# Performance work log

Hardware: AMD Instinct MI355X
Metric: run time of the kernel (lower is better)

The kernel has to match this reference:

```python
import jax, jax.numpy as jnp
import numpy as np

LAYER_SPECS = [(2, 4, 1), (2, 4, 1), (1, 4, 1), (1, 4, 1)]
SKIPS = [(k - s) * d for (s, k, d) in LAYER_SPECS]  # (ksz-stride)*dilation
C = 80  # encoder channels


def _conv1d(x, w, b, stride, dilation):
    # x: (N, Cin, L), w: (Cout, Cin, K)
    out = jax.lax.conv_general_dilated(
        x, w, window_strides=(stride,), padding='VALID',
        rhs_dilation=(dilation,), dimension_numbers=('NCH', 'OIH', 'NCH'))
    return out + b[None, :, None]


def _encoder(x, w_wide, b_wide, w_1x1, b_1x1, w_f0, b_f0, w_f1, b_f1):
    # x: (N, T, 80) -> (N, T', 80)
    x = jnp.transpose(x, (0, 2, 1))  # (N, 80, T)
    for i, ((stride, ksz, dil), skip) in enumerate(zip(LAYER_SPECS, SKIPS)):
        x1 = _conv1d(x, w_wide[i], b_wide[i], stride, dil)  # (N, 2C, L')
        a, g = jnp.split(x1, 2, axis=1)
        x2 = jnp.tanh(a) * jax.nn.sigmoid(g)                # gated activation
        x3 = _conv1d(x2, w_1x1[i], b_1x1[i], 1, 1)          # (N, C, L')
        if i == 0:
            x = x3
        else:
            T3 = x3.shape[2]
            # residual: strided slice of previous x, take last of each stride group
            res = x[:, :, skip:skip + T3 * stride].reshape(x.shape[0], C, T3, stride)[:, :, :, -1]
            x = x3 + res
    x = _conv1d(jax.nn.relu(_conv1d(x, w_f0, b_f0, 1, 1)), w_f1, b_f1, 1, 1)
    return jnp.transpose(x, (0, 2, 1))  # (N, T', 80)


def setup_inputs() -> dict:
    key = jax.random.key(0)
    ks = jax.random.split(key, 10)
    N, Ts, Tq = 16, 8192, 2048
    return {
        'search': jax.random.normal(ks[0], (N, Ts, 80), dtype=jnp.float32),
        'query': jax.random.normal(ks[1], (N, Tq, 80), dtype=jnp.float32),
        'w_wide': jax.random.normal(ks[2], (4, 160, 80, 4), dtype=jnp.float32) * 0.02,
        'b_wide': jnp.zeros((4, 160), dtype=jnp.float32),
        'w_1x1': jax.random.normal(ks[3], (4, 80, 80, 1), dtype=jnp.float32) * 0.05,
        'b_1x1': jnp.zeros((4, 80), dtype=jnp.float32),
        'w_f0': jax.random.normal(ks[4], (80, 80, 1), dtype=jnp.float32) * 0.05,
        'b_f0': jnp.zeros((80,), dtype=jnp.float32),
        'w_f1': jax.random.normal(ks[5], (80, 80, 1), dtype=jnp.float32) * 0.05,
        'b_f1': jax.random.normal(ks[6], (80,), dtype=jnp.float32) * 0.05,
        'embedding': jax.random.normal(ks[7], (1, 512, 80), dtype=jnp.float32) * 0.001,
        'w_lin': jax.random.normal(ks[8], (2, 80), dtype=jnp.float32) * 0.05,
        'b_lin': jnp.zeros((2,), dtype=jnp.float32),
    }


def reference(search, query, w_wide, b_wide, w_1x1, b_1x1,
              w_f0, b_f0, w_f1, b_f1, embedding, w_lin, b_lin):
    enc_s = _encoder(search, w_wide, b_wide, w_1x1, b_1x1, w_f0, b_f0, w_f1, b_f1)
    enc_q = _encoder(query, w_wide, b_wide, w_1x1, b_1x1, w_f0, b_f0, w_f1, b_f1)

    # ---- VectorQuant (no normalize): nearest-codeword lookup + straight-through ----
    x = enc_s[:, :, None, :]                  # (N, T, 1, V)
    N, T, nc, V = x.shape
    n_classes = embedding.shape[1]
    x1 = x.reshape(N * T, nc, V)              # (NT, 1, V)
    # squared-distance via expansion: argmin identical to argmin of L2 norm
    x2 = jnp.sum(x1 * x1, axis=-1, keepdims=True)          # (NT, 1, 1)
    e2 = jnp.sum(embedding * embedding, axis=-1)[None]     # (1, 1, K)
    xe = jnp.einsum('ncv,ckv->nck', x1, embedding)         # (NT, 1, K)
    idx = jnp.argmin(x2 - 2.0 * xe + e2, axis=2)           # (NT, 1)
    offset = jnp.arange(nc) * n_classes
    flat = embedding.reshape(-1, V)
    output = flat[(idx + offset[None, :]).reshape(-1)].reshape(x.shape)
    out0 = jax.lax.stop_gradient(output - x) + x           # straight-through
    discrete = out0[:, :, 0, :]               # (N, Ts', V)

    # ---- align query to search length, classify, max-pool over time ----
    sf = discrete.shape[1] // enc_q.shape[1]
    q = jnp.tile(enc_q, (1, sf, 1))
    pad = discrete.shape[1] - q.shape[1]
    q = jnp.pad(q, ((0, 0), (0, pad), (0, 0)))
    pred = jnp.tanh((q + discrete) @ w_lin.T + b_lin)      # (N, Ts', 2)
    return jnp.max(pred, axis=1)                           # (N, 2)
```

## Files before the change

kernel.cpp:

```cpp
#include <hip/hip_runtime.h>
#include <math.h>


#define NBATCH 16

typedef __attribute__((ext_vector_type(8))) short s16x8;
typedef __attribute__((ext_vector_type(4))) float f32x4;

__device__ __forceinline__ float fast_sigmoid(float x){ return 1.0f/(1.0f+__expf(-x)); }
__device__ __forceinline__ float fast_tanh(float x){ return 2.0f/(1.0f+__expf(-2.0f*x))-1.0f; }
__device__ __forceinline__ unsigned short f2bf(float f){
    unsigned int u = __float_as_uint(f);
    return (unsigned short)((u + 0x7FFFu + ((u >> 16) & 1u)) >> 16);
}

__global__ __launch_bounds__(256) void pack_all(
    const float* __restrict__ w_wide, const float* __restrict__ w_1x1,
    const float* __restrict__ wf0,    const float* __restrict__ wf1,
    const float* __restrict__ emb,
    unsigned short* __restrict__ WW, unsigned short* __restrict__ W1,
    unsigned short* __restrict__ F0, unsigned short* __restrict__ F1,
    unsigned short* __restrict__ EM, float* __restrict__ e2o)
{
    int i = blockIdx.x * 256 + threadIdx.x;
    if (i < 204800) {
        int l = i / 51200, r = i % 51200, oc = r / 320, k = r % 320;
        int j = k / 80, ic = k % 80;
        WW[i] = f2bf(w_wide[l * 51200 + oc * 320 + ic * 4 + j]);
    } else if (i < 235520) {
        int idx = i - 204800, l = idx / 7680, r = idx % 7680, oc = r / 96, k = r % 96;
        W1[idx] = (k < 80) ? f2bf(w_1x1[l * 6400 + oc * 80 + k]) : (unsigned short)0;
    } else if (i < 243200) {
        int idx = i - 235520, oc = idx / 96, k = idx % 96;
        F0[idx] = (k < 80) ? f2bf(wf0[oc * 80 + k]) : (unsigned short)0;
    } else if (i < 250880) {
        int idx = i - 243200, oc = idx / 96, k = idx % 96;
        F1[idx] = (k < 80) ? f2bf(wf1[oc * 80 + k]) : (unsigned short)0;
    } else if (i < 291840) {
        EM[i - 250880] = f2bf(emb[i - 250880]);
    } else if (i < 292352) {
        int e = i - 291840;
        float s = 0.f;
        for (int k = 0; k < 80; ++k) { float v = emb[e * 80 + k]; s = fmaf(v, v, s); }
        e2o[e] = s;
    }
}

template<int S, bool HAS_RES, bool FINAL>
__global__ __launch_bounds__(320, 6) void enc_layer(
    const float* __restrict__ xS, const float* __restrict__ xQ,
    const unsigned short* __restrict__ ww,  const float* __restrict__ wb,
    const unsigned short* __restrict__ w1p, const float* __restrict__ b1,
    const unsigned short* __restrict__ f0p, const float* __restrict__ bf0,
    const unsigned short* __restrict__ f1p, const float* __restrict__ bf1,
    float* __restrict__ outS, float* __restrict__ outQ,
    int TinS, int ToutS, int TinQ, int ToutQ, int nbS)
{
    constexpr int TILE = 32;
    constexpr int MT   = 2;
    constexpr int P    = (TILE - 1) * S + 4;
    constexpr int HALF = (S == 2) ? (P / 2) : P;
    constexpr int NEL  = P * 20;
    constexpr int NST  = (NEL + 319) / 320;
    constexpr int NPARY = (S == 2) ? 2 : 1;

    __shared__ __attribute__((aligned(16))) unsigned short xs[NPARY * HALF * 88];
    __shared__ __attribute__((aligned(16))) unsigned short gsA[TILE * 104];
    __shared__ __attribute__((aligned(16))) unsigned short gsB[FINAL ? TILE * 104 : 8];

    const int tid  = threadIdx.x;
    const int wave = tid >> 6;
    const int lane = tid & 63;
    const int m    = lane & 15;
    const int quad = lane >> 4;
    const int n_   = blockIdx.y;

    const float* x; float* out; int T_in, T_out, bx;
    if ((int)blockIdx.x < nbS) { x = xS; out = outS; T_in = TinS; T_out = ToutS; bx = blockIdx.x; }
    else                       { x = xQ; out = outQ; T_in = TinQ; T_out = ToutQ; bx = blockIdx.x - nbS; }
    const int t0 = bx * TILE;
    const long base_in = (long)n_ * T_in * 80;

    const int quad8 = quad * 8;
    const unsigned short* wa_base = ww + (long)(wave * 16 + m) * 320 + quad8;
    const unsigned short* wg_base = ww + (long)((wave + 5) * 16 + m) * 320 + quad8;
    auto ldB = [&](const unsigned short* b, int kk) { return *(const s16x8*)(b + kk * 32); };

    float4 vst[NST]; int odx[NST]; bool okw[NST];
#pragma unroll
    for (int it = 0; it < NST; ++it) {
        int u = tid + it * 320;
        okw[it] = (u < NEL);
        if (u >= NEL) u = NEL - 1;
        int pos = u / 20, c4 = u % 20;
        int tp = t0 * S + pos; if (tp > T_in - 1) tp = T_in - 1;
        vst[it] = *(const float4*)(x + base_in + (long)tp * 80 + c4 * 4);
        int row = (S == 2) ? (pos >> 1) : pos;
        int par = (S == 2) ? (pos & 1) : 0;
        odx[it] = (par * HALF + row) * 88 + c4 * 4;
    }

    s16x8 baP[3], bgP[3];
    baP[0] = ldB(wa_base, 0); bgP[0] = ldB(wg_base, 0);
    baP[1] = ldB(wa_base, 1); bgP[1] = ldB(wg_base, 1);

#pragma unroll
    for (int it = 0; it < NST; ++it) {
        if (okw[it]) {
            float4 v = vst[it];
            unsigned int s0 = (unsigned int)f2bf(v.x) | ((unsigned int)f2bf(v.y) << 16);
            unsigned int s1 = (unsigned int)f2bf(v.z) | ((unsigned int)f2bf(v.w) << 16);
            *(uint2*)&xs[odx[it]] = make_uint2(s0, s1);
        }
    }

    f32x4 acc_a[MT], acc_g[MT];
#pragma unroll
    for (int mt = 0; mt < MT; ++mt) {
        acc_a[mt] = (f32x4){0.f, 0.f, 0.f, 0.f};
        acc_g[mt] = (f32x4){0.f, 0.f, 0.f, 0.f};
    }

    __syncthreads();

#pragma unroll
    for (int kk = 0; kk < 10; ++kk) {
        if (kk + 2 < 10) {
            baP[(kk + 2) % 3] = ldB(wa_base, kk + 2);
            bgP[(kk + 2) % 3] = ldB(wg_base, kk + 2);
        }
        const int kq = kk * 32 + quad8;
        const int j  = (kq >= 240) ? 3 : ((kq >= 160) ? 2 : ((kq >= 80) ? 1 : 0));
        const int ic0 = kq - j * 80;
        int xb;
        if (S == 2) xb = ((j & 1) * HALF + (j >> 1)) * 88 + ic0;
        else        xb = j * 88 + ic0;
        s16x8 a[MT];
#pragma unroll
        for (int mt = 0; mt < MT; ++mt)
            a[mt] = *(const s16x8*)&xs[xb + (mt * 16 + m) * 88];
        s16x8 ba = baP[kk % 3], bg = bgP[kk % 3];
#pragma unroll
        for (int mt = 0; mt < MT; ++mt) {
            acc_a[mt] = __builtin_amdgcn_mfma_f32_16x16x32_bf16(a[mt], ba, acc_a[mt], 0, 0, 0);
            acc_g[mt] = __builtin_amdgcn_mfma_f32_16x16x32_bf16(a[mt], bg, acc_g[mt], 0, 0, 0);
        }
    }

    const float ba_b = wb[wave * 16 + m];
    const float bg_b = wb[80 + wave * 16 + m];
#pragma unroll
    for (int mt = 0; mt < MT; ++mt)
#pragma unroll
        for (int r = 0; r < 4; ++r) {
            float av = acc_a[mt][r] + ba_b;
            float gv = acc_g[mt][r] + bg_b;
            gsA[(mt * 16 + quad * 4 + r) * 104 + wave * 16 + m] =
                f2bf(fast_tanh(av) * fast_sigmoid(gv));
        }
    const uint4 z4 = make_uint4(0u, 0u, 0u, 0u);
    {
        constexpr int NPAD = FINAL ? 128 : 64;
        for (int u = tid; u < NPAD; u += 320) {
            unsigned short* g = (u < 64) ? gsA : gsB;
            int v = u & 63;
            *(uint4*)&g[(v >> 1) * 104 + 80 + (v & 1) * 8] = z4;
        }
    }
    __syncthreads();

    auto mm96 = [&](const unsigned short* Wp, const unsigned short* g, f32x4 (&o)[MT]) {
        const unsigned short* wb1 = Wp + (long)(wave * 16 + m) * 96 + quad8;
        s16x8 b0  = *(const s16x8*)(wb1);
        s16x8 b1f = *(const s16x8*)(wb1 + 32);
        s16x8 b2  = *(const s16x8*)(wb1 + 64);
#pragma unroll
        for (int mt = 0; mt < MT; ++mt) o[mt] = (f32x4){0.f, 0.f, 0.f, 0.f};
#pragma unroll
        for (int kb = 0; kb < 3; ++kb) {
            s16x8 b = (kb == 0) ? b0 : ((kb == 1) ? b1f : b2);
#pragma unroll
            for (int mt = 0; mt < MT; ++mt) {
                s16x8 ag = *(const s16x8*)&g[(mt * 16 + m) * 104 + kb * 32 + quad8];
                o[mt] = __builtin_amdgcn_mfma_f32_16x16x32_bf16(ag, b, o[mt], 0, 0, 0);
            }
        }
    };

    f32x4 a1[MT];
    mm96(w1p, gsA, a1);

    const long base_out = (long)n_ * T_out * 80;
    const int c = wave * 16 + m;
    if (!FINAL) {
        const float b1c = b1[c];
#pragma unroll
        for (int mt = 0; mt < MT; ++mt)
#pragma unroll
            for (int r = 0; r < 4; ++r) {
                int tg = t0 + mt * 16 + quad * 4 + r;
                if (tg < T_out) {
                    float v = a1[mt][r] + b1c;
                    if (HAS_RES)
                        v += x[base_in + (long)(3 + (long)tg * S) * 80 + c];
                    out[base_out + (long)tg * 80 + c] = v;
                }
            }
    } else {
        const float b1c = b1[c];
        float x3[MT][4];
#pragma unroll
        for (int mt = 0; mt < MT; ++mt)
#pragma unroll
            for (int r = 0; r < 4; ++r) {
                int tg = t0 + mt * 16 + quad * 4 + r;
                int tc = (tg < T_out) ? tg : (T_out - 1);
                float v = a1[mt][r] + b1c;
                if (HAS_RES)
                    v += x[base_in + (long)(3 + (long)tc * S) * 80 + c];
                x3[mt][r] = v;
            }
#pragma unroll
        for (int mt = 0; mt < MT; ++mt)
#pragma unroll
            for (int r = 0; r < 4; ++r)
                gsB[(mt * 16 + quad * 4 + r) * 104 + c] = f2bf(x3[mt][r]);
        __syncthreads();
        f32x4 a2[MT];
        mm96(f0p, gsB, a2);
        const float bf0c = bf0[c];
#pragma unroll
        for (int mt = 0; mt < MT; ++mt)
#pragma unroll
            for (int r = 0; r < 4; ++r)
                gsA[(mt * 16 + quad * 4 + r) * 104 + c] =
                    f2bf(fmaxf(a2[mt][r] + bf0c, 0.f));
        __syncthreads();
        f32x4 a3[MT];
        mm96(f1p, gsA, a3);
        const float bf1c = bf1[c];
#pragma unroll
        for (int mt = 0; mt < MT; ++mt)
#pragma unroll
            for (int r = 0; r < 4; ++r) {
                int tg = t0 + mt * 16 + quad * 4 + r;
                if (tg < T_out)
                    out[base_out + (long)tg * 80 + c] = a3[mt][r] + bf1c;
            }
    }
}

__global__ __launch_bounds__(256, 2) void vq_mfma(
    const float* __restrict__ enc_s, const float* __restrict__ enc_q,
    const unsigned short* __restrict__ embp, const float* __restrict__ emb,
    const float* __restrict__ e2v,
    const float* __restrict__ w_lin, const float* __restrict__ b_lin,
    float* __restrict__ pred)
{
    __shared__ unsigned short xs[64 * 104];
    __shared__ unsigned short es[128 * 104];
    const uint4 z4 = make_uint4(0u, 0u, 0u, 0u);

    const int tid  = threadIdx.x;
    const int wave = tid >> 6;
    const int lane = tid & 63;
    const int m    = lane & 15;
    const int quad = lane >> 4;
    const int n    = blockIdx.y;
    const int t0   = blockIdx.x * 64;

    for (int u = tid; u < 64 * 20; u += 256) {
        int row = u / 20, c4 = u % 20;
        int t = t0 + row; if (t > 2039) t = 2039;
        float4 v = *(const float4*)(enc_s + ((long)n * 2040 + t) * 80 + c4 * 4);
        unsigned int s0 = (unsigned int)f2bf(v.x) | ((unsigned int)f2bf(v.y) << 16);
        unsigned int s1 = (unsigned int)f2bf(v.z) | ((unsigned int)f2bf(v.w) << 16);
        *(uint2*)&xs[row * 104 + c4 * 4] = make_uint2(s0, s1);
    }
    for (int u = tid; u < 128; u += 256)
        *(uint4*)&xs[(u >> 1) * 104 + 80 + (u & 1) * 8] = z4;
    __syncthreads();

    s16x8 af[3];
#pragma unroll
    for (int kb = 0; kb < 3; ++kb)
        af[kb] = *(const s16x8*)&xs[(wave * 16 + m) * 104 + kb * 32 + quad * 8];

    float best[4]; int bi[4];
#pragma unroll
    for (int r = 0; r < 4; ++r) { best[r] = 1e30f; bi[r] = 0; }

    for (int ch = 0; ch < 4; ++ch) {
        const int c0 = ch * 128;
        __syncthreads();
        for (int u = tid; u < 128 * 12; u += 256) {
            int el = u / 12, seg = u % 12;
            uint4 v = z4;
            if (seg < 10) v = *(const uint4*)(embp + (long)(c0 + el) * 80 + seg * 8);
            *(uint4*)&es[el * 104 + seg * 8] = v;
        }
        __syncthreads();

        f32x4 acc[8];
#pragma unroll
        for (int nt = 0; nt < 8; ++nt) acc[nt] = (f32x4){0.f, 0.f, 0.f, 0.f};
#pragma unroll
        for (int kb = 0; kb < 3; ++kb) {
            const int k0 = kb * 32 + quad * 8;
#pragma unroll
            for (int nt = 0; nt < 8; ++nt) {
                s16x8 b = *(const s16x8*)&es[(nt * 16 + m) * 104 + k0];
                acc[nt] = __builtin_amdgcn_mfma_f32_16x16x32_bf16(af[kb], b, acc[nt], 0, 0, 0);
            }
        }
#pragma unroll
        for (int nt = 0; nt < 8; ++nt) {
            const int e = c0 + nt * 16 + m;
            const float e2x = e2v[e];
#pragma unroll
            for (int r = 0; r < 4; ++r) {
                float s = fmaf(-2.0f, acc[nt][r], e2x);
                if (s < best[r]) { best[r] = s; bi[r] = e; }
            }
        }
    }

    __syncthreads();
    float* rb = (float*)es;
    int*   ri = (int*)es + 1088;
#pragma unroll
    for (int r = 0; r < 4; ++r) {
        int tl = wave * 16 + quad * 4 + r;
        rb[tl * 17 + m] = best[r];
        ri[tl * 17 + m] = bi[r];
    }
    __syncthreads();

    if (tid < 64) {
        const int t = t0 + tid;
        float b = rb[tid * 17]; int ix = ri[tid * 17];
#pragma unroll
        for (int j = 1; j < 16; ++j) {
            float v = rb[tid * 17 + j]; int iv = ri[tid * 17 + j];
            if (v < b || (v == b && iv < ix)) { b = v; ix = iv; }
        }
        if (t < 2040) {
            const float4* ev = (const float4*)(emb + (long)ix * 80);
            const bool hasq = (t < 2016);
            const float4* qv = hasq
                ? (const float4*)(enc_q + ((long)n * 504 + (t % 504)) * 80) : nullptr;
            float p0 = b_lin[0], p1 = b_lin[1];
#pragma unroll
            for (int i = 0; i < 20; ++i) {
                float4 e4 = ev[i];
                float4 q4 = hasq ? qv[i] : make_float4(0.f, 0.f, 0.f, 0.f);
                float4 w0 = *(const float4*)(w_lin + 4 * i);
                float4 w1 = *(const float4*)(w_lin + 80 + 4 * i);
                float sx = e4.x + q4.x, sy = e4.y + q4.y;
                float sz = e4.z + q4.z, sw = e4.w + q4.w;
                p0 = fmaf(sx, w0.x, p0); p1 = fmaf(sx, w1.x, p1);
                p0 = fmaf(sy, w0.y, p0); p1 = fmaf(sy, w1.y, p1);
                p0 = fmaf(sz, w0.z, p0); p1 = fmaf(sz, w1.z, p1);
                p0 = fmaf(sw, w0.w, p0); p1 = fmaf(sw, w1.w, p1);
            }
            long o = ((long)n * 2040 + t) * 2;
            pred[o]     = fast_tanh(p0);
            pred[o + 1] = fast_tanh(p1);
        }
    }
}

__global__ __launch_bounds__(256) void max_red(const float* __restrict__ pred,
                                               float* __restrict__ out)
{
    __shared__ float s0[256], s1[256];
    const int n = blockIdx.x, tid = threadIdx.x;
    float m0 = -1e30f, m1 = -1e30f;
    for (int t = tid; t < 2040; t += 256) {
        long o = ((long)n * 2040 + t) * 2;
        m0 = fmaxf(m0, pred[o]);
        m1 = fmaxf(m1, pred[o + 1]);
    }
    s0[tid] = m0; s1[tid] = m1;
    __syncthreads();
    for (int st = 128; st > 0; st >>= 1) {
        if (tid < st) {
            s0[tid] = fmaxf(s0[tid], s0[tid + st]);
            s1[tid] = fmaxf(s1[tid], s1[tid + st]);
        }
        __syncthreads();
    }
    if (tid == 0) { out[n * 2] = s0[0]; out[n * 2 + 1] = s1[0]; }
}

extern "C" void kernel_launch(void* const* d_in, const int* in_sizes, int n_in,
                              void* d_out, int out_size, void* d_ws, size_t ws_size,
                              hipStream_t stream)
{
    const float* search = (const float*)d_in[0];
    const float* query  = (const float*)d_in[1];
    const float* w_wide = (const float*)d_in[2];
    const float* b_wide = (const float*)d_in[3];
    const float* w_1x1  = (const float*)d_in[4];
    const float* b_1x1  = (const float*)d_in[5];
    const float* w_f0   = (const float*)d_in[6];
    const float* b_f0   = (const float*)d_in[7];
    const float* w_f1   = (const float*)d_in[8];
    const float* b_f1   = (const float*)d_in[9];
    const float* emb    = (const float*)d_in[10];
    const float* w_lin  = (const float*)d_in[11];
    const float* b_lin  = (const float*)d_in[12];
    float* out = (float*)d_out;
    float* ws  = (float*)d_ws;

    float* A  = ws;
    float* B  = A  + 5241600;
    float* C  = B  + 2618880;
    float* QA = C  + 2618880;
    float* QB = QA + 1309440;
    float* QC = QB + 652800;
    unsigned short* WWp = (unsigned short*)(QC + 652800);
    unsigned short* W1p = WWp + 204800;
    unsigned short* F0p = W1p + 30720;
    unsigned short* F1p = F0p + 7680;
    unsigned short* EMp = F1p + 7680;
    float* e2b = (float*)(EMp + 40960);

    const dim3 blk(320);
    auto nb = [](int T) { return (T + 31) / 32; };

    pack_all<<<dim3(1142), dim3(256), 0, stream>>>(w_wide, w_1x1, w_f0, w_f1, emb,
                                                   WWp, W1p, F0p, F1p, EMp, e2b);

    enc_layer<2, false, false><<<dim3(nb(4095) + nb(1023), NBATCH), blk, 0, stream>>>(
        search, query, WWp, b_wide, W1p, b_1x1, nullptr, nullptr, nullptr, nullptr,
        A, QA, 8192, 4095, 2048, 1023, nb(4095));
    enc_layer<2, true, false><<<dim3(nb(2046) + nb(510), NBATCH), blk, 0, stream>>>(
        A, QA, WWp + 51200, b_wide + 160, W1p + 7680, b_1x1 + 80,
        nullptr, nullptr, nullptr, nullptr,
        B, QB, 4095, 2046, 1023, 510, nb(2046));
    enc_layer<1, true, false><<<dim3(nb(2043) + nb(507), NBATCH), blk, 0, stream>>>(
        B, QB, WWp + 102400, b_wide + 320, W1p + 15360, b_1x1 + 160,
        nullptr, nullptr, nullptr, nullptr,
        C, QC, 2046, 2043, 510, 507, nb(2043));
    enc_layer<1, true, true><<<dim3(nb(2040) + nb(504), NBATCH), blk, 0, stream>>>(
        C, QC, WWp + 153600, b_wide + 480, W1p + 23040, b_1x1 + 240,
        F0p, b_f0, F1p, b_f1,
        B, QB, 2043, 2040, 507, 504, nb(2040));

    vq_mfma<<<dim3(32, NBATCH), dim3(256), 0, stream>>>(B, QB, EMp, emb, e2b,
                                                        w_lin, b_lin, C);
    max_red<<<dim3(NBATCH), dim3(256), 0, stream>>>(C, out);
}
```

Measured before the change: 240.8 us.

## Double encoder time tile and keep all layer weights resident in registers

Raises the encoder tile from 32 to 64 output timesteps (MT 4), preloads all ten wide-conv weight fragments plus the 1x1 and final conv weights into registers up front, widens the shared-memory row stride to 104, and converts to bf16 with a packed hardware instruction. The aim is to halve the number of blocks, reuse each weight load over more timesteps, and cut repeated global weight fetches inside the MFMA loop. In exchange, register pressure rises sharply, occupancy is lowered to 2 blocks per CU via launch bounds, and there are fewer blocks to spread across the GPU.

```diff
diff --git a/kernel.cpp b/kernel.cpp
--- a/kernel.cpp
+++ b/kernel.cpp
@@ -12,6 +12,11 @@
 __device__ __forceinline__ unsigned short f2bf(float f){
     unsigned int u = __float_as_uint(f);
     return (unsigned short)((u + 0x7FFFu + ((u >> 16) & 1u)) >> 16);
+}
+__device__ __forceinline__ unsigned int pk2bf(float lo, float hi){
+    unsigned int r;
+    asm("v_cvt_pk_bf16_f32 %0, %1, %2" : "=v"(r) : "v"(lo), "v"(hi));
+    return r;
 }
 
 __global__ __launch_bounds__(256) void pack_all(
@@ -47,7 +52,7 @@
 }
 
 template<int S, bool HAS_RES, bool FINAL>
-__global__ __launch_bounds__(320, 6) void enc_layer(
+__global__ __launch_bounds__(320, 2) void enc_layer(
     const float* __restrict__ xS, const float* __restrict__ xQ,
     const unsigned short* __restrict__ ww,  const float* __restrict__ wb,
     const unsigned short* __restrict__ w1p, const float* __restrict__ b1,
@@ -56,15 +61,16 @@
     float* __restrict__ outS, float* __restrict__ outQ,
     int TinS, int ToutS, int TinQ, int ToutQ, int nbS)
 {
-    constexpr int TILE = 32;
-    constexpr int MT   = 2;
-    constexpr int P    = (TILE - 1) * S + 4;
-    constexpr int HALF = (S == 2) ? (P / 2) : P;
+    constexpr int TILE = 64;
+    constexpr int MT   = 4;
+    constexpr int P    = 63 * S + 4;
+    constexpr int HALF = (S == 2) ? 65 : 67;
+    constexpr int NPARY = (S == 2) ? 2 : 1;
+    constexpr int XSTR = 104;
     constexpr int NEL  = P * 20;
     constexpr int NST  = (NEL + 319) / 320;
-    constexpr int NPARY = (S == 2) ? 2 : 1;
-
-    __shared__ __attribute__((aligned(16))) unsigned short xs[NPARY * HALF * 88];
+
+    __shared__ __attribute__((aligned(16))) unsigned short xs[NPARY * HALF * XSTR];
     __shared__ __attribute__((aligned(16))) unsigned short gsA[TILE * 104];
     __shared__ __attribute__((aligned(16))) unsigned short gsB[FINAL ? TILE * 104 : 8];
 
@@ -80,11 +86,6 @@
     else                       { x = xQ; out = outQ; T_in = TinQ; T_out = ToutQ; bx = blockIdx.x - nbS; }
     const int t0 = bx * TILE;
     const long base_in = (long)n_ * T_in * 80;
-
-    const int quad8 = quad * 8;
-    const unsigned short* wa_base = ww + (long)(wave * 16 + m) * 320 + quad8;
-    const unsigned short* wg_base = ww + (long)((wave + 5) * 16 + m) * 320 + quad8;
-    auto ldB = [&](const unsigned short* b, int kk) { return *(const s16x8*)(b + kk * 32); };
 
     float4 vst[NST]; int odx[NST]; bool okw[NST];
 #pragma unroll
@@ -97,20 +98,32 @@
         vst[it] = *(const float4*)(x + base_in + (long)tp * 80 + c4 * 4);
         int row = (S == 2) ? (pos >> 1) : pos;
         int par = (S == 2) ? (pos & 1) : 0;
-        odx[it] = (par * HALF + row) * 88 + c4 * 4;
-    }
-
-    s16x8 baP[3], bgP[3];
-    baP[0] = ldB(wa_base, 0); bgP[0] = ldB(wg_base, 0);
-    baP[1] = ldB(wa_base, 1); bgP[1] = ldB(wg_base, 1);
+        odx[it] = (par * HALF + row) * XSTR + c4 * 4;
+    }
+
+    const int quad8 = quad * 8;
+    const unsigned short* wa_base = ww + (long)(wave * 16 + m) * 320 + quad8;
+    const unsigned short* wg_base = ww + (long)((wave + 5) * 16 + m) * 320 + quad8;
+    s16x8 wA[10], wG[10];
+#pragma unroll
+    for (int kk = 0; kk < 10; ++kk) {
+        wA[kk] = *(const s16x8*)(wa_base + kk * 32);
+        wG[kk] = *(const s16x8*)(wg_base + kk * 32);
+    }
+    const unsigned short* wb1 = w1p + (long)(wave * 16 + m) * 96 + quad8;
+    s16x8 w1b0 = *(const s16x8*)(wb1);
+    s16x8 w1b1 = *(const s16x8*)(wb1 + 32);
+    s16x8 w1b2 = *(const s16x8*)(wb1 + 64);
+    const float ba_b = wb[wave * 16 + m];
+    const float bg_b = wb[80 + wave * 16 + m];
+    const int c = wave * 16 + m;
+    const float b1c = b1[c];
 
 #pragma unroll
     for (int it = 0; it < NST; ++it) {
         if (okw[it]) {
             float4 v = vst[it];
-            unsigned int s0 = (unsigned int)f2bf(v.x) | ((unsigned int)f2bf(v.y) << 16);
-            unsigned int s1 = (unsigned int)f2bf(v.z) | ((unsigned int)f2bf(v.w) << 16);
-            *(uint2*)&xs[odx[it]] = make_uint2(s0, s1);
+            *(uint2*)&xs[odx[it]] = make_uint2(pk2bf(v.x, v.y), pk2bf(v.z, v.w));
         }
     }
 
@@ -125,55 +138,44 @@
 
 #pragma unroll
     for (int kk = 0; kk < 10; ++kk) {
-        if (kk + 2 < 10) {
-            baP[(kk + 2) % 3] = ldB(wa_base, kk + 2);
-            bgP[(kk + 2) % 3] = ldB(wg_base, kk + 2);
-        }
         const int kq = kk * 32 + quad8;
         const int j  = (kq >= 240) ? 3 : ((kq >= 160) ? 2 : ((kq >= 80) ? 1 : 0));
         const int ic0 = kq - j * 80;
         int xb;
-        if (S == 2) xb = ((j & 1) * HALF + (j >> 1)) * 88 + ic0;
-        else        xb = j * 88 + ic0;
+        if (S == 2) xb = ((j & 1) * HALF + (j >> 1)) * XSTR + ic0;
+        else        xb = j * XSTR + ic0;
         s16x8 a[MT];
 #pragma unroll
         for (int mt = 0; mt < MT; ++mt)
-            a[mt] = *(const s16x8*)&xs[xb + (mt * 16 + m) * 88];
-        s16x8 ba = baP[kk % 3], bg = bgP[kk % 3];
+            a[mt] = *(const s16x8*)&xs[xb + (mt * 16 + m) * XSTR];
 #pragma unroll
         for (int mt = 0; mt < MT; ++mt) {
-            acc_a[mt] = __builtin_amdgcn_mfma_f32_16x16x32_bf16(a[mt], ba, acc_a[mt], 0, 0, 0);
-            acc_g[mt] = __builtin_amdgcn_mfma_f32_16x16x32_bf16(a[mt], bg, acc_g[mt], 0, 0, 0);
-        }
-    }
-
-    const float ba_b = wb[wave * 16 + m];
-    const float bg_b = wb[80 + wave * 16 + m];
+            acc_a[mt] = __builtin_amdgcn_mfma_f32_16x16x32_bf16(a[mt], wA[kk], acc_a[mt], 0, 0, 0);
+            acc_g[mt] = __builtin_amdgcn_mfma_f32_16x16x32_bf16(a[mt], wG[kk], acc_g[mt], 0, 0, 0);
+        }
+    }
+
 #pragma unroll
     for (int mt = 0; mt < MT; ++mt)
 #pragma unroll
         for (int r = 0; r < 4; ++r) {
             float av = acc_a[mt][r] + ba_b;
             float gv = acc_g[mt][r] + bg_b;
-            gsA[(mt * 16 + quad * 4 + r) * 104 + wave * 16 + m] =
+            gsA[(mt * 16 + quad * 4 + r) * 104 + c] =
                 f2bf(fast_tanh(av) * fast_sigmoid(gv));
         }
     const uint4 z4 = make_uint4(0u, 0u, 0u, 0u);
     {
-        constexpr int NPAD = FINAL ? 128 : 64;
+        constexpr int NPAD = FINAL ? 256 : 128;
         for (int u = tid; u < NPAD; u += 320) {
-            unsigned short* g = (u < 64) ? gsA : gsB;
-            int v = u & 63;
+            unsigned short* g = (u < 128) ? gsA : gsB;
+            int v = u & 127;
             *(uint4*)&g[(v >> 1) * 104 + 80 + (v & 1) * 8] = z4;
         }
     }
     __syncthreads();
 
-    auto mm96 = [&](const unsigned short* Wp, const unsigned short* g, f32x4 (&o)[MT]) {
-        const unsigned short* wb1 = Wp + (long)(wave * 16 + m) * 96 + quad8;
-        s16x8 b0  = *(const s16x8*)(wb1);
-        s16x8 b1f = *(const s16x8*)(wb1 + 32);
-        s16x8 b2  = *(const s16x8*)(wb1 + 64);
+    auto mm96 = [&](s16x8 b0, s16x8 b1f, s16x8 b2, const unsigned short* g, f32x4 (&o)[MT]) {
 #pragma unroll
         for (int mt = 0; mt < MT; ++mt) o[mt] = (f32x4){0.f, 0.f, 0.f, 0.f};
 #pragma unroll
@@ -188,12 +190,10 @@
     };
 
     f32x4 a1[MT];
-    mm96(w1p, gsA, a1);
+    mm96(w1b0, w1b1, w1b2, gsA, a1);
 
     const long base_out = (long)n_ * T_out * 80;
-    const int c = wave * 16 + m;
     if (!FINAL) {
-        const float b1c = b1[c];
 #pragma unroll
         for (int mt = 0; mt < MT; ++mt)
 #pragma unroll
@@ -207,7 +207,6 @@
                 }
             }
     } else {
-        const float b1c = b1[c];
         float x3[MT][4];
 #pragma unroll
         for (int mt = 0; mt < MT; ++mt)
@@ -220,6 +219,11 @@
                     v += x[base_in + (long)(3 + (long)tc * S) * 80 + c];
                 x3[mt][r] = v;
             }
+        const unsigned short* wf0b = f0p + (long)c * 96 + quad8;
+        s16x8 f0b0 = *(const s16x8*)(wf0b);
+        s16x8 f0b1 = *(const s16x8*)(wf0b + 32);
+        s16x8 f0b2 = *(const s16x8*)(wf0b + 64);
+        const float bf0c = bf0[c];
 #pragma unroll
         for (int mt = 0; mt < MT; ++mt)
 #pragma unroll
@@ -227,8 +231,12 @@
                 gsB[(mt * 16 + quad * 4 + r) * 104 + c] = f2bf(x3[mt][r]);
         __syncthreads();
         f32x4 a2[MT];
-        mm96(f0p, gsB, a2);
-        const float bf0c = bf0[c];
+        mm96(f0b0, f0b1, f0b2, gsB, a2);
+        const unsigned short* wf1b = f1p + (long)c * 96 + quad8;
+        s16x8 f1b0 = *(const s16x8*)(wf1b);
+        s16x8 f1b1 = *(const s16x8*)(wf1b + 32);
+        s16x8 f1b2 = *(const s16x8*)(wf1b + 64);
+        const float bf1c = bf1[c];
 #pragma unroll
         for (int mt = 0; mt < MT; ++mt)
 #pragma unroll
@@ -237,8 +245,7 @@
                     f2bf(fmaxf(a2[mt][r] + bf0c, 0.f));
         __syncthreads();
         f32x4 a3[MT];
-        mm96(f1p, gsA, a3);
-        const float bf1c = bf1[c];
+        mm96(f1b0, f1b1, f1b2, gsA, a3);
 #pragma unroll
         for (int mt = 0; mt < MT; ++mt)
 #pragma unroll
@@ -427,7 +434,7 @@
     float* e2b = (float*)(EMp + 40960);
 
     const dim3 blk(320);
-    auto nb = [](int T) { return (T + 31) / 32; };
+    auto nb = [](int T) { return (T + 63) / 64; };
 
     pack_all<<<dim3(1142), dim3(256), 0, stream>>>(w_wide, w_1x1, w_f0, w_f1, emb,
                                                    WWp, W1p, F0p, F1p, EMp, e2b);
```

Result: slower. 267.4 us (+11.0%).
